# Optimization experiments

Hardware: AMD Instinct MI355X
Metric: run time of the kernel (lower is better)

Reference implementation:

```python
import jax, jax.numpy as jnp
import numpy as np

N = 50000        # num nodes
IN = 128         # in_features
H = 4            # num heads
C = 32           # out features per head (out_features // num_heads, concat_heads=True)
E_RAND = 450000  # random edges (plus N self-loops -> E = 500000)
ALPHA = 0.2      # LeakyReLU negative slope


def setup_inputs() -> dict:
    key = jax.random.key(0)
    k1, k2, k3, k4 = jax.random.split(key, 4)
    x = jax.random.normal(k1, (N, IN), jnp.float32)
    # xavier_uniform-ish scale with gain 1.414 (std = gain*sqrt(2/(fan_in+fan_out)))
    W = jax.random.normal(k2, (H * C, IN), jnp.float32) * (1.414 * np.sqrt(2.0 / (IN + H * C)))
    b = jnp.zeros((H * C,), jnp.float32)
    a = jax.random.normal(k3, (H, 2 * C), jnp.float32) * (1.414 * np.sqrt(2.0 / (H + 2 * C)))
    # self-loops guarantee every source node has >=1 edge, so the edge-wise
    # segment softmax matches the dense masked softmax of the original module.
    self_loops = jnp.stack([jnp.arange(N, dtype=jnp.int32)] * 2, axis=1)
    rand_edges = jax.random.randint(k4, (E_RAND, 2), 0, N, jnp.int32)
    edges = jnp.concatenate([self_loops, rand_edges], axis=0)  # (E, 2) = (src, dst)
    return {"x": x, "W": W, "b": b, "a": a, "edges": edges}


def reference(x, W, b, a, edges):
    num_nodes = x.shape[0]
    # projection: (N, IN) -> (N, H, C)
    h = (x @ W.T + b).reshape(num_nodes, H, C)
    src, dst = edges[:, 0], edges[:, 1]
    hs = h[src]  # (E, H, C) gather of source node feats
    hd = h[dst]  # (E, H, C) gather of destination node feats
    a_input = jnp.concatenate([hs, hd], axis=-1)  # (E, H, 2C)
    logits = jnp.einsum('ehc,hc->eh', a_input, a)
    logits = jax.nn.leaky_relu(logits, ALPHA)
    # segment softmax over outgoing edges of each source node (== dense masked
    # softmax over dim=2 in the original, given every node has >=1 out-edge)
    m = jax.lax.stop_gradient(jax.ops.segment_max(logits, src, num_segments=num_nodes))
    ex = jnp.exp(logits - m[src])
    denom = jax.ops.segment_sum(ex, src, num_segments=num_nodes)
    probs = ex / denom[src]  # (E, H)
    # weighted scatter-aggregate of destination feats into source nodes
    out = jax.ops.segment_sum(probs[..., None] * hd, src, num_segments=num_nodes)  # (N, H, C)
    return out.reshape(1, num_nodes, H * C)  # concat_heads=True, batch_size=1
```

## Files before the change

### kernel.cpp

```cpp
#include <hip/hip_runtime.h>
#include <math.h>

#define LRELU_ALPHA 0.2f
#define CAP 64

typedef __attribute__((ext_vector_type(8))) short bf16x8;
typedef __attribute__((ext_vector_type(4))) float f32x4;

__device__ __forceinline__ void split2(float f0, float f1, unsigned& hi, unsigned& lo) {
    unsigned u0 = __float_as_uint(f0), u1 = __float_as_uint(f1);
    unsigned h0 = u0 & 0xFFFF0000u, h1 = u1 & 0xFFFF0000u;
    float l0f = f0 - __uint_as_float(h0);
    float l1f = f1 - __uint_as_float(h1);
    hi = (h0 >> 16) | h1;
    lo = (__float_as_uint(l0f) >> 16) | (__float_as_uint(l1f) & 0xFFFF0000u);
}
__device__ __forceinline__ unsigned short f2bf(float f) {
    unsigned u = __float_as_uint(f);
    return (unsigned short)((u + 0x7FFFu + ((u >> 16) & 1u)) >> 16);
}
__device__ __forceinline__ float bf2f(unsigned short s) {
    return __uint_as_float(((unsigned)s) << 16);
}

__global__ __launch_bounds__(256) void k_init(const float* __restrict__ W,
                                              bf16x8* __restrict__ wf,
                                              int* __restrict__ cnt, int N) {
    int i = blockIdx.x * 256 + threadIdx.x;
    if (i < N) cnt[i] = 0;
    if (blockIdx.x < 8) {
        int id = i;
        int lane = id & 63, ks = (id >> 6) & 3, ct = id >> 8;
        int j = ct * 16 + (lane & 15);
        int k0 = ks * 32 + ((lane >> 4) << 3);
        const float* wp = W + j * 128 + k0;
        float4 f0 = *reinterpret_cast<const float4*>(wp);
        float4 f1 = *reinterpret_cast<const float4*>(wp + 4);
        uint4 hv, lv;
        split2(f0.x, f0.y, hv.x, lv.x);
        split2(f0.z, f0.w, hv.y, lv.y);
        split2(f1.x, f1.y, hv.z, lv.z);
        split2(f1.z, f1.w, hv.w, lv.w);
        *reinterpret_cast<uint4*>(&wf[id]) = hv;
        *reinterpret_cast<uint4*>(&wf[2048 + id]) = lv;
    }
}

__global__ __launch_bounds__(256) void k_gemm(const float* __restrict__ x,
                                              const bf16x8* __restrict__ wf,
                                              const float* __restrict__ b,
                                              const float* __restrict__ a,
                                              unsigned short* __restrict__ hb,
                                              float* __restrict__ asrc,
                                              float* __restrict__ adst, int N,
                                              const int* __restrict__ edges,
                                              int* __restrict__ cnt,
                                              int* __restrict__ col, int E) {
    __shared__ __align__(16) unsigned char sXH[32 * 256];
    __shared__ __align__(16) unsigned char sXL[32 * 256];
    const int t = threadIdx.x;
    const int w = t >> 6;
    const int l = t & 63;
    const int base = blockIdx.x * 32;

    for (int e = blockIdx.x * 256 + t; e < E; e += gridDim.x * 256) {
        int2 ed = *reinterpret_cast<const int2*>(&edges[(size_t)e * 2]);
        int pos = atomicAdd(&cnt[ed.x], 1);
        if (pos < CAP) col[ed.x * CAP + pos] = ed.y;
    }

    bf16x8 wh[2][4], wl[2][4];
    #pragma unroll
    for (int ctl = 0; ctl < 2; ++ctl)
        #pragma unroll
        for (int ks = 0; ks < 4; ++ks) {
            int fid = (((2 * w + ctl) * 4 + ks) << 6) + l;
            wh[ctl][ks] = wf[fid];
            wl[ctl][ks] = wf[2048 + fid];
        }

    int jj[2];
    float bv[2], asw[2], adw[2];
    #pragma unroll
    for (int ctl = 0; ctl < 2; ++ctl) {
        jj[ctl] = w * 32 + ctl * 16 + (l & 15);
        bv[ctl] = b[jj[ctl]];
        asw[ctl] = a[w * 64 + ctl * 16 + (l & 15)];
        adw[ctl] = a[w * 64 + 32 + ctl * 16 + (l & 15)];
    }

    #pragma unroll
    for (int i = 0; i < 4; ++i) {
        int f = t + i * 256;
        int r = f >> 5, c4 = f & 31;
        int gr = base + r;
        float4 v = (gr < N) ? *reinterpret_cast<const float4*>(x + (size_t)gr * 128 + c4 * 4)
                            : make_float4(0.f, 0.f, 0.f, 0.f);
        unsigned h01, h23, l01, l23;
        split2(v.x, v.y, h01, l01);
        split2(v.z, v.w, h23, l23);
        int boff = r * 256 + ((c4 * 8) ^ ((r & 7) << 4));
        *reinterpret_cast<uint2*>(sXH + boff) = make_uint2(h01, h23);
        *reinterpret_cast<uint2*>(sXL + boff) = make_uint2(l01, l23);
    }
    __syncthreads();

    f32x4 acc[2][2];
    #pragma unroll
    for (int rt = 0; rt < 2; ++rt)
        #pragma unroll
        for (int ctl = 0; ctl < 2; ++ctl)
            acc[rt][ctl] = (f32x4){0.f, 0.f, 0.f, 0.f};

    #pragma unroll
    for (int ks = 0; ks < 4; ++ks) {
        #pragma unroll
        for (int rt = 0; rt < 2; ++rt) {
            int r = rt * 16 + (l & 15);
            int boff = r * 256 + (((ks * 64) + ((l >> 4) << 4)) ^ ((r & 7) << 4));
            bf16x8 xh = *reinterpret_cast<const bf16x8*>(sXH + boff);
            bf16x8 xl = *reinterpret_cast<const bf16x8*>(sXL + boff);
            #pragma unroll
            for (int ctl = 0; ctl < 2; ++ctl) {
                acc[rt][ctl] = __builtin_amdgcn_mfma_f32_16x16x32_bf16(xh, wh[ctl][ks], acc[rt][ctl], 0, 0, 0);
                acc[rt][ctl] = __builtin_amdgcn_mfma_f32_16x16x32_bf16(xh, wl[ctl][ks], acc[rt][ctl], 0, 0, 0);
                acc[rt][ctl] = __builtin_amdgcn_mfma_f32_16x16x32_bf16(xl, wh[ctl][ks], acc[rt][ctl], 0, 0, 0);
            }
        }
    }

    #pragma unroll
    for (int rt = 0; rt < 2; ++rt) {
        #pragma unroll
        for (int reg = 0; reg < 4; ++reg) {
            int n = base + rt * 16 + ((l >> 4) << 2) + reg;
            bool ok = (n < N);
            float v0 = acc[rt][0][reg] + bv[0];
            float v1 = acc[rt][1][reg] + bv[1];
            if (ok) {
                hb[(size_t)n * 128 + jj[0]] = f2bf(v0);
                hb[(size_t)n * 128 + jj[1]] = f2bf(v1);
            }
            float ps = v0 * asw[0] + v1 * asw[1];
            float pd = v0 * adw[0] + v1 * adw[1];
            #pragma unroll
            for (int mask = 1; mask <= 8; mask <<= 1) {
                ps += __shfl_xor(ps, mask);
                pd += __shfl_xor(pd, mask);
            }
            if (ok && (l & 15) == 0) {
                asrc[n * 4 + w] = ps;
                adst[n * 4 + w] = pd;
            }
        }
    }
}

__global__ __launch_bounds__(256) void k_node(const int* __restrict__ cnt,
                                              const int* __restrict__ col,
                                              const float* __restrict__ asrc,
                                              const float* __restrict__ adst,
                                              const unsigned short* __restrict__ hb,
                                              float* __restrict__ out, int N) {
    int n = blockIdx.x * 8 + (threadIdx.x >> 5);
    if (n >= N) return;
    int l = threadIdx.x & 31;
    int hd = l >> 3;
    float asr = asrc[n * 4 + hd];
    int deg = min(cnt[n], CAP);
    const int* cp = col + n * CAP;
    float ax = 0.f, ay = 0.f, az = 0.f, aw = 0.f, den = 0.f;
    int k = 0;
    for (; k + 8 <= deg; k += 8) {
        int c[8];
        #pragma unroll
        for (int u = 0; u < 8; ++u) c[u] = cp[k + u];
        float ev[8];
        #pragma unroll
        for (int u = 0; u < 8; ++u) {
            float g = asr + adst[c[u] * 4 + hd];
            g = (g >= 0.f) ? g : LRELU_ALPHA * g;
            ev[u] = __expf(g);
        }
        #pragma unroll
        for (int u = 0; u < 8; ++u) {
            ushort4 q = *reinterpret_cast<const ushort4*>(&hb[(size_t)c[u] * 128 + l * 4]);
            ax += ev[u] * bf2f(q.x); ay += ev[u] * bf2f(q.y);
            az += ev[u] * bf2f(q.z); aw += ev[u] * bf2f(q.w);
            den += ev[u];
        }
    }
    for (; k < deg; ++k) {
        int c = cp[k];
        float g = asr + adst[c * 4 + hd];
        g = (g >= 0.f) ? g : LRELU_ALPHA * g;
        float e = __expf(g);
        ushort4 q = *reinterpret_cast<const ushort4*>(&hb[(size_t)c * 128 + l * 4]);
        ax += e * bf2f(q.x); ay += e * bf2f(q.y); az += e * bf2f(q.z); aw += e * bf2f(q.w);
        den += e;
    }
    float inv = 1.f / den;
    *reinterpret_cast<float4*>(&out[(size_t)n * 128 + l * 4]) =
        make_float4(ax * inv, ay * inv, az * inv, aw * inv);
}

extern "C" void kernel_launch(void* const* d_in, const int* in_sizes, int n_in,
                              void* d_out, int out_size, void* d_ws, size_t ws_size,
                              hipStream_t stream) {
    const float* x = (const float*)d_in[0];
    const float* W = (const float*)d_in[1];
    const float* b = (const float*)d_in[2];
    const float* a = (const float*)d_in[3];
    const int* edges = (const int*)d_in[4];
    const int N = in_sizes[0] / 128;
    const int E = in_sizes[4] / 2;
    float* out = (float*)d_out;

    char* ws = (char*)d_ws;
    unsigned short* hb = (unsigned short*)ws; ws += (size_t)N * 128 * 2;
    float* asrc = (float*)ws;     ws += (size_t)N * 4 * 4;
    float* adst = (float*)ws;     ws += (size_t)N * 4 * 4;
    int* cnt = (int*)ws;          ws += (size_t)N * 4;
    int* col = (int*)ws;          ws += (size_t)N * CAP * 4;
    bf16x8* wf = (bf16x8*)ws;     ws += (size_t)4096 * 16;

    const int nb = (N + 255) / 256;
    hipLaunchKernelGGL(k_init, dim3(nb), dim3(256), 0, stream, W, wf, cnt, N);
    hipLaunchKernelGGL(k_gemm, dim3((N + 31) / 32), dim3(256), 0, stream,
                       x, wf, b, a, hb, asrc, adst, N, edges, cnt, col, E);
    hipLaunchKernelGGL(k_node, dim3((N + 7) / 8), dim3(256), 0, stream,
                       cnt, col, asrc, adst, hb, out, N);
}
```

Baseline: 78.16 us.

## Load x fragments directly from global memory, dropping LDS staging in GEMM

The GEMM kernel no longer stages the x tile into shared memory as split bf16 hi/lo halves behind a block barrier. Each wave now loads its own MFMA operand fragments straight from global memory and splits them into hi/lo bf16 in registers. This removes the LDS writes, the __syncthreads and the LDS reads. In exchange, the four waves each reload the same x rows (4x redundant global/L2 traffic) and redo the split conversion.

```diff
diff --git a/kernel.cpp b/kernel.cpp
--- a/kernel.cpp
+++ b/kernel.cpp
@@ -22,6 +22,8 @@
 __device__ __forceinline__ float bf2f(unsigned short s) {
     return __uint_as_float(((unsigned)s) << 16);
 }
+
+union bfpack { unsigned u[4]; bf16x8 v; };
 
 __global__ __launch_bounds__(256) void k_init(const float* __restrict__ W,
                                               bf16x8* __restrict__ wf,
@@ -56,8 +58,6 @@
                                               const int* __restrict__ edges,
                                               int* __restrict__ cnt,
                                               int* __restrict__ col, int E) {
-    __shared__ __align__(16) unsigned char sXH[32 * 256];
-    __shared__ __align__(16) unsigned char sXL[32 * 256];
     const int t = threadIdx.x;
     const int w = t >> 6;
     const int l = t & 63;
@@ -89,22 +89,6 @@
         adw[ctl] = a[w * 64 + 32 + ctl * 16 + (l & 15)];
     }
 
-    #pragma unroll
-    for (int i = 0; i < 4; ++i) {
-        int f = t + i * 256;
-        int r = f >> 5, c4 = f & 31;
-        int gr = base + r;
-        float4 v = (gr < N) ? *reinterpret_cast<const float4*>(x + (size_t)gr * 128 + c4 * 4)
-                            : make_float4(0.f, 0.f, 0.f, 0.f);
-        unsigned h01, h23, l01, l23;
-        split2(v.x, v.y, h01, l01);
-        split2(v.z, v.w, h23, l23);
-        int boff = r * 256 + ((c4 * 8) ^ ((r & 7) << 4));
-        *reinterpret_cast<uint2*>(sXH + boff) = make_uint2(h01, h23);
-        *reinterpret_cast<uint2*>(sXL + boff) = make_uint2(l01, l23);
-    }
-    __syncthreads();
-
     f32x4 acc[2][2];
     #pragma unroll
     for (int rt = 0; rt < 2; ++rt)
@@ -113,18 +97,26 @@
             acc[rt][ctl] = (f32x4){0.f, 0.f, 0.f, 0.f};
 
     #pragma unroll
-    for (int ks = 0; ks < 4; ++ks) {
-        #pragma unroll
-        for (int rt = 0; rt < 2; ++rt) {
-            int r = rt * 16 + (l & 15);
-            int boff = r * 256 + (((ks * 64) + ((l >> 4) << 4)) ^ ((r & 7) << 4));
-            bf16x8 xh = *reinterpret_cast<const bf16x8*>(sXH + boff);
-            bf16x8 xl = *reinterpret_cast<const bf16x8*>(sXL + boff);
+    for (int rt = 0; rt < 2; ++rt) {
+        int r = base + rt * 16 + (l & 15);
+        bool rok = (r < N);
+        const float* xp = x + (size_t)r * 128 + ((l >> 4) << 3);
+        #pragma unroll
+        for (int ks = 0; ks < 4; ++ks) {
+            float4 f0 = rok ? *reinterpret_cast<const float4*>(xp + ks * 32)
+                            : make_float4(0.f, 0.f, 0.f, 0.f);
+            float4 f1 = rok ? *reinterpret_cast<const float4*>(xp + ks * 32 + 4)
+                            : make_float4(0.f, 0.f, 0.f, 0.f);
+            bfpack xh, xl;
+            split2(f0.x, f0.y, xh.u[0], xl.u[0]);
+            split2(f0.z, f0.w, xh.u[1], xl.u[1]);
+            split2(f1.x, f1.y, xh.u[2], xl.u[2]);
+            split2(f1.z, f1.w, xh.u[3], xl.u[3]);
             #pragma unroll
             for (int ctl = 0; ctl < 2; ++ctl) {
-                acc[rt][ctl] = __builtin_amdgcn_mfma_f32_16x16x32_bf16(xh, wh[ctl][ks], acc[rt][ctl], 0, 0, 0);
-                acc[rt][ctl] = __builtin_amdgcn_mfma_f32_16x16x32_bf16(xh, wl[ctl][ks], acc[rt][ctl], 0, 0, 0);
-                acc[rt][ctl] = __builtin_amdgcn_mfma_f32_16x16x32_bf16(xl, wh[ctl][ks], acc[rt][ctl], 0, 0, 0);
+                acc[rt][ctl] = __builtin_amdgcn_mfma_f32_16x16x32_bf16(xh.v, wh[ctl][ks], acc[rt][ctl], 0, 0, 0);
+                acc[rt][ctl] = __builtin_amdgcn_mfma_f32_16x16x32_bf16(xh.v, wl[ctl][ks], acc[rt][ctl], 0, 0, 0);
+                acc[rt][ctl] = __builtin_amdgcn_mfma_f32_16x16x32_bf16(xl.v, wh[ctl][ks], acc[rt][ctl], 0, 0, 0);
             }
         }
     }
```

Result: slower. 85.80 us (+9.8%).
